# Kernel tuning notes

Measured on AMD Instinct MI355X. Metric: run time of the kernel, lower is better.

Reference implementation:

```python
import jax, jax.numpy as jnp
import numpy as np

N_HEADS = 16
D_MODEL = 1024
NEG_INF = float('-inf')


def _rope_tables(seq_len, d_k, dtype):
    # RoPE(dim=d_k//2): Theta_i = 10000^(-i/dim), repeat-interleaved to width d_k;
    # positions start at 1 (torch uses arange(1, max_len+1)).
    dim = d_k // 2
    theta = jnp.exp(-jnp.arange(dim, dtype=dtype) * (np.log(10000.0) / dim))
    theta = jnp.repeat(theta, 2)                      # [d_k]
    pos = jnp.arange(1, seq_len + 1, dtype=dtype)[:, None]  # [S,1]
    ang = pos * theta                                 # [S,d_k]
    return jnp.sin(ang), jnp.cos(ang)


def _rope(x):
    # x: [B,H,S,d_k]; pair rotation (x0,x1)->(-x1,x0), Rx = x*cos + rot(x)*sin
    B, H, S, d_k = x.shape
    sin, cos = _rope_tables(S, d_k, x.dtype)
    xp = x.reshape(B, H, S, d_k // 2, 2)
    rot = jnp.stack([-xp[..., 1], xp[..., 0]], axis=-1).reshape(x.shape)
    return x * cos + rot * sin


def setup_inputs() -> dict:
    key = jax.random.key(0)
    ks = jax.random.split(key, 8)
    B, S, D, H = 2, 1024, D_MODEL, N_HEADS
    source_query = jax.random.normal(ks[0], (B, S, D), dtype=jnp.float32)
    source_key_value = jax.random.normal(ks[1], (B, S, D), dtype=jnp.float32)
    # tail padding: lengths in [820, 1024]
    q_len = jax.random.randint(ks[2], (B,), 820, S + 1)
    kv_len = jax.random.randint(ks[3], (B,), 820, S + 1)
    pos = jnp.arange(S)
    source_query_padding_mask = pos[None, :] >= q_len[:, None]    # True = pad
    source_key_value_padding_mask = pos[None, :] >= kv_len[:, None]
    prev = jax.random.normal(ks[4], (1, B, H, S, S), dtype=jnp.float32) * 0.5
    Wq = jax.random.normal(ks[5], (D, D), dtype=jnp.float32) * 0.02
    Wk = jax.random.normal(ks[6], (D, D), dtype=jnp.float32) * 0.02
    kv2 = jax.random.split(ks[7], 2)
    Wv = jax.random.normal(kv2[0], (D, D), dtype=jnp.float32) * 0.02
    Wproj = jax.random.normal(kv2[1], (D, D), dtype=jnp.float32) * 0.02
    return dict(source_query=source_query, source_key_value=source_key_value,
                source_query_padding_mask=source_query_padding_mask,
                source_key_value_padding_mask=source_key_value_padding_mask,
                prev=prev, Wq=Wq, Wk=Wk, Wv=Wv, Wproj=Wproj)


def reference(source_query, source_key_value, source_query_padding_mask,
              source_key_value_padding_mask, prev, Wq, Wk, Wv, Wproj):
    B, Sq, D = source_query.shape
    Sk = source_key_value.shape[1]
    H = N_HEADS
    d_k = D // H

    def split_heads(x, S):
        return x.reshape(B, S, H, d_k).transpose(0, 2, 1, 3)  # [B,H,S,d_k]

    # nn.Linear(bias=False): y = x @ W.T
    q = split_heads(jnp.einsum('bsd,ed->bse', source_query, Wq), Sq)
    k = split_heads(jnp.einsum('bsd,ed->bse', source_key_value, Wk), Sk)
    v = split_heads(jnp.einsum('bsd,ed->bse', source_key_value, Wv), Sk)

    q = _rope(q)
    k = _rope(k)

    scores = jnp.einsum('bhqd,bhkd->bhqk', q, k) * (d_k ** -0.5)
    q_pad = source_query_padding_mask[:, None, :, None]   # [B,1,Sq,1]
    kv_pad = source_key_value_padding_mask[:, None, None, :]  # [B,1,1,Sk]
    scores = jnp.where(q_pad, NEG_INF, scores)
    scores = jnp.where(kv_pad, NEG_INF, scores)
    causal = jnp.tril(jnp.ones((Sq, Sq), dtype=bool))      # masked=True
    scores = jnp.where(causal, scores, NEG_INF)

    prev_new = jnp.concatenate([prev, scores[None]], axis=0)  # [L+1,B,H,Sq,Sk]
    avg = prev_new.mean(0)

    # rows fully -inf (padded queries) would softmax to NaN in torch, then get
    # filled with 0 -> compute a safe softmax and zero those rows instead.
    safe = jnp.where(q_pad, 0.0, avg)
    w = jax.nn.softmax(safe, axis=-1)
    w = jnp.where(q_pad, 0.0, w)

    attn = jnp.einsum('bhqk,bhkd->bhqd', w, v)
    attn = attn.transpose(0, 2, 1, 3).reshape(B, Sq, D)
    out = jnp.einsum('bsd,ed->bse', attn, Wproj)  # dropout=0 (eval)
    return out, prev_new
```

## Files before the change

### kernel.cpp

```cpp
#include <hip/hip_runtime.h>
#include <math.h>

#define NSEQ 1024
#define NH   16
#define DKH  64

#define NEGBIG (-1.0e30f)

__global__ __launch_bounds__(256) void normalize_masks(
    const unsigned char* __restrict__ qm, const unsigned char* __restrict__ km,
    int* __restrict__ outq, int* __restrict__ outk)
{
    __shared__ int flag;
    if (threadIdx.x == 0) flag = 0;
    __syncthreads();
    int f = 0;
    for (int i = threadIdx.x; i < 2048; i += 256) {
        if ((i & 3) && qm[i]) f = 1;
        if ((i & 3) && km[i]) f = 1;
    }
    if (f) atomicOr(&flag, 1);
    __syncthreads();
    const int isbyte = flag;
    for (int i = threadIdx.x; i < 2048; i += 256) {
        outq[i] = isbyte ? (int)qm[i] : ((const int*)qm)[i];
        outk[i] = isbyte ? (int)km[i] : ((const int*)km)[i];
    }
}

__device__ __forceinline__ void gemm_core(
    const float* __restrict__ X, const float* __restrict__ W,
    float (*As)[68], float (*Bs)[132], float (&acc)[8][4],
    int m0, int e0, int tid)
{
    const int tm = tid >> 5, tn = tid & 31;
    const int arow = tid >> 2, akq = (tid & 3) * 4;
    const int brow = tid >> 1, bkq = (tid & 1) * 8;
    const float* aptr = &X[(size_t)(m0 + arow) * 1024 + akq];
    const float* bptr = &W[(size_t)(e0 + brow) * 1024 + bkq];

    float4 ar  = *(const float4*)aptr;
    float4 br0 = *(const float4*)bptr;
    float4 br1 = *(const float4*)(bptr + 4);

    for (int k0 = 0; k0 < 1024; k0 += 16) {
        As[akq + 0][arow] = ar.x;  As[akq + 1][arow] = ar.y;
        As[akq + 2][arow] = ar.z;  As[akq + 3][arow] = ar.w;
        Bs[bkq + 0][brow] = br0.x; Bs[bkq + 1][brow] = br0.y;
        Bs[bkq + 2][brow] = br0.z; Bs[bkq + 3][brow] = br0.w;
        Bs[bkq + 4][brow] = br1.x; Bs[bkq + 5][brow] = br1.y;
        Bs[bkq + 6][brow] = br1.z; Bs[bkq + 7][brow] = br1.w;
        __syncthreads();
        if (k0 + 16 < 1024) {
            ar  = *(const float4*)(aptr + k0 + 16);
            br0 = *(const float4*)(bptr + k0 + 16);
            br1 = *(const float4*)(bptr + k0 + 16 + 4);
        }
        #pragma unroll
        for (int k = 0; k < 16; ++k) {
            float a[8], bb[4];
            *(float4*)&a[0]  = *(const float4*)&As[k][tm * 8];
            *(float4*)&a[4]  = *(const float4*)&As[k][tm * 8 + 4];
            *(float4*)&bb[0] = *(const float4*)&Bs[k][tn * 4];
            #pragma unroll
            for (int i = 0; i < 8; ++i)
                #pragma unroll
                for (int j = 0; j < 4; ++j)
                    acc[i][j] += a[i] * bb[j];
        }
        __syncthreads();
    }
}

__global__ __launch_bounds__(256) void gemm_qkv(
    const float* __restrict__ srcq, const float* __restrict__ srckv,
    const float* __restrict__ Wq, const float* __restrict__ Wk,
    const float* __restrict__ Wv,
    float* __restrict__ qh, float* __restrict__ kh, float* __restrict__ vh)
{
    __shared__ float As[16][68];
    __shared__ float Bs[16][132];
    const int tid = threadIdx.x;
    const int z = blockIdx.z;
    const float* X = (z == 0) ? srcq : srckv;
    const float* W = (z == 0) ? Wq : (z == 1) ? Wk : Wv;
    float* Y       = (z == 0) ? qh : (z == 1) ? kh : vh;
    const int m0 = blockIdx.y * 64, e0 = blockIdx.x * 128;

    float acc[8][4] = {{0.f}};
    gemm_core(X, W, As, Bs, acc, m0, e0, tid);

    const int tm = tid >> 5, tn = tid & 31;
    const int col = e0 + tn * 4;
    const int h = col >> 6, dbase = col & 63;
    const bool rope = (z != 2);
    float th0 = 0.f, th1 = 0.f;
    if (rope) {
        const float cth = 0.28782313662425575f;
        th0 = expf(-(float)(dbase >> 1) * cth);
        th1 = expf(-(float)((dbase >> 1) + 1) * cth);
    }
    #pragma unroll
    for (int i = 0; i < 8; ++i) {
        const int m = m0 + tm * 8 + i;
        const int b = m >> 10, s = m & 1023;
        float v0 = acc[i][0], v1 = acc[i][1], v2 = acc[i][2], v3 = acc[i][3];
        if (rope) {
            const float pos = (float)(s + 1);
            float s0, c0, s1, c1;
            sincosf(pos * th0, &s0, &c0);
            sincosf(pos * th1, &s1, &c1);
            float r0 = v0 * c0 - v1 * s0;
            float r1 = v1 * c0 + v0 * s0;
            float r2 = v2 * c1 - v3 * s1;
            float r3 = v3 * c1 + v2 * s1;
            v0 = r0; v1 = r1; v2 = r2; v3 = r3;
        }
        const size_t idx = (((size_t)(b * NH + h) << 10) + s) * DKH + dbase;
        *(float4*)&Y[idx] = make_float4(v0, v1, v2, v3);
    }
}

__global__ __launch_bounds__(256) void gemm_proj(
    const float* __restrict__ X, const float* __restrict__ W,
    float* __restrict__ Y)
{
    __shared__ float As[16][68];
    __shared__ float Bs[16][132];
    const int tid = threadIdx.x;
    const int m0 = blockIdx.y * 64, e0 = blockIdx.x * 128;
    float acc[8][4] = {{0.f}};
    gemm_core(X, W, As, Bs, acc, m0, e0, tid);
    const int tm = tid >> 5, tn = tid & 31;
    #pragma unroll
    for (int i = 0; i < 8; ++i)
        *(float4*)&Y[(size_t)(m0 + tm * 8 + i) * 1024 + e0 + tn * 4] =
            make_float4(acc[i][0], acc[i][1], acc[i][2], acc[i][3]);
}

__global__ __launch_bounds__(256) void flash_fused(
    const float* __restrict__ qh, const float* __restrict__ kh,
    const float* __restrict__ vh, const float* __restrict__ prev,
    const int* __restrict__ nmq, const int* __restrict__ nmk,
    float* __restrict__ prevc, float* __restrict__ scb,
    float* __restrict__ attn)
{
    const int bh = blockIdx.y;
    const int b = bh >> 4, h = bh & 15;
    const int bx = blockIdx.x;
    const int qt = (bx & 1) ? (15 - (bx >> 1)) : (bx >> 1);
    const int q0 = qt * 64;
    const int tid = threadIdx.x;
    const int ti = tid >> 4, tj = tid & 15;
    const int r0 = ti * 4, c0 = tj * 4;
    const size_t base = ((size_t)bh << 10) * 1024;
    const float NI = NEGBIG;

    __shared__ float Qs[64][68];
    __shared__ float KW[64][68];
    __shared__ float Vs[64][68];

    const int lr = tid >> 2;
    const int ld0 = (tid & 3) * 4;
    {
        const float* qbase = qh + (((size_t)bh << 10) + q0) * DKH;
        #pragma unroll
        for (int dq = 0; dq < 4; ++dq) {
            const int d0 = ld0 + dq * 16;
            float4 qv = *(const float4*)&qbase[(size_t)lr * DKH + d0];
            Qs[d0 + 0][lr] = qv.x; Qs[d0 + 1][lr] = qv.y;
            Qs[d0 + 2][lr] = qv.z; Qs[d0 + 3][lr] = qv.w;
        }
    }

    {
        const float4 ninf4 = make_float4(NI, NI, NI, NI);
        for (int kt = qt + 1; kt < 16; ++kt) {
            const int k0 = kt * 64;
            #pragma unroll
            for (int u = 0; u < 4; ++u) {
                const int e = u * 256 + tid;
                const int rr = e >> 4, cc = (e & 15) * 4;
                const size_t idx = base + (size_t)(q0 + rr) * 1024 + k0 + cc;
                *(float4*)&prevc[idx] = *(const float4*)&prev[idx];
                *(float4*)&scb[idx] = ninf4;
            }
        }
    }

    int qmv[4];
    #pragma unroll
    for (int i = 0; i < 4; ++i) qmv[i] = nmq[(b << 10) + q0 + r0 + i];

    float m_i[4], l_i[4], O[4][4];
    #pragma unroll
    for (int i = 0; i < 4; ++i) {
        m_i[i] = -3.0e38f; l_i[i] = 0.f;
        #pragma unroll
        for (int j = 0; j < 4; ++j) O[i][j] = 0.f;
    }

    const float* kbase = kh + ((size_t)bh << 10) * DKH;
    const float* vbase = vh + ((size_t)bh << 10) * DKH;

    for (int kt = 0; kt <= qt; ++kt) {
        const int k0 = kt * 64;
        __syncthreads();

        #pragma unroll
        for (int dq = 0; dq < 4; ++dq) {
            const int d0 = ld0 + dq * 16;
            float4 kv4 = *(const float4*)&kbase[(size_t)(k0 + lr) * DKH + d0];
            KW[d0 + 0][lr] = kv4.x; KW[d0 + 1][lr] = kv4.y;
            KW[d0 + 2][lr] = kv4.z; KW[d0 + 3][lr] = kv4.w;
        }
        #pragma unroll
        for (int u = 0; u < 4; ++u) {
            const int e = u * 256 + tid;
            const int kv = e >> 4, dd = (e & 15) * 4;
            *(float4*)&Vs[kv][dd] =
                *(const float4*)&vbase[(size_t)(k0 + kv) * DKH + dd];
        }
        __syncthreads();

        float acc[4][4] = {{0.f}};
        #pragma unroll 8
        for (int d = 0; d < 64; ++d) {
            float a[4], bb[4];
            *(float4*)a  = *(const float4*)&Qs[d][r0];
            *(float4*)bb = *(const float4*)&KW[d][c0];
            #pragma unroll
            for (int i = 0; i < 4; ++i)
                #pragma unroll
                for (int j = 0; j < 4; ++j)
                    acc[i][j] += a[i] * bb[j];
        }

        int km[4];
        #pragma unroll
        for (int j = 0; j < 4; ++j) km[j] = nmk[(b << 10) + k0 + c0 + j];
        float aw[4][4], tmx[4];
        #pragma unroll
        for (int i = 0; i < 4; ++i) {
            const int row = q0 + r0 + i;
            float o[4];
            #pragma unroll
            for (int j = 0; j < 4; ++j) {
                const int col = k0 + c0 + j;
                const bool masked = (col > row) || (qmv[i] != 0) || (km[j] != 0);
                o[j] = masked ? NI : acc[i][j] * 0.125f;
            }
            const size_t idx = base + (size_t)row * 1024 + k0 + c0;
            *(float4*)&scb[idx] = make_float4(o[0], o[1], o[2], o[3]);
            const float4 p4 = *(const float4*)&prev[idx];
            *(float4*)&prevc[idx] = p4;
            aw[i][0] = 0.5f * (p4.x + o[0]);
            aw[i][1] = 0.5f * (p4.y + o[1]);
            aw[i][2] = 0.5f * (p4.z + o[2]);
            aw[i][3] = 0.5f * (p4.w + o[3]);
            tmx[i] = fmaxf(fmaxf(aw[i][0], aw[i][1]), fmaxf(aw[i][2], aw[i][3]));
        }
        #pragma unroll
        for (int i = 0; i < 4; ++i)
            #pragma unroll
            for (int off = 1; off < 16; off <<= 1)
                tmx[i] = fmaxf(tmx[i], __shfl_xor(tmx[i], off));

        __syncthreads();

        #pragma unroll
        for (int i = 0; i < 4; ++i) {
            const float mn = fmaxf(m_i[i], tmx[i]);
            const float fac = expf(m_i[i] - mn);
            m_i[i] = mn;
            float w0 = expf(aw[i][0] - mn);
            float w1 = expf(aw[i][1] - mn);
            float w2 = expf(aw[i][2] - mn);
            float w3 = expf(aw[i][3] - mn);
            float sl = w0 + w1 + w2 + w3;
            #pragma unroll
            for (int off = 1; off < 16; off <<= 1)
                sl += __shfl_xor(sl, off);
            l_i[i] = l_i[i] * fac + sl;
            #pragma unroll
            for (int j = 0; j < 4; ++j) O[i][j] *= fac;
            KW[c0 + 0][r0 + i] = w0;
            KW[c0 + 1][r0 + i] = w1;
            KW[c0 + 2][r0 + i] = w2;
            KW[c0 + 3][r0 + i] = w3;
        }
        __syncthreads();

        #pragma unroll 8
        for (int k = 0; k < 64; ++k) {
            float wv[4], vv[4];
            *(float4*)wv = *(const float4*)&KW[k][r0];
            *(float4*)vv = *(const float4*)&Vs[k][c0];
            #pragma unroll
            for (int i = 0; i < 4; ++i)
                #pragma unroll
                for (int j = 0; j < 4; ++j)
                    O[i][j] += wv[i] * vv[j];
        }
    }

    #pragma unroll
    for (int i = 0; i < 4; ++i) {
        const int q = q0 + r0 + i;
        const float inv = qmv[i] ? 0.f : 1.f / l_i[i];
        float4 o4 = make_float4(O[i][0] * inv, O[i][1] * inv,
                                O[i][2] * inv, O[i][3] * inv);
        *(float4*)&attn[(size_t)((b << 10) + q) * 1024 + (h << 6) + c0] = o4;
    }
}

extern "C" void kernel_launch(void* const* d_in, const int* in_sizes, int n_in,
                              void* d_out, int out_size, void* d_ws, size_t ws_size,
                              hipStream_t stream) {
    const float* srcq  = (const float*)d_in[0];
    const float* srckv = (const float*)d_in[1];
    const void*  qmask = d_in[2];
    const void*  kmask = d_in[3];
    const float* prev  = (const float*)d_in[4];
    const float* Wq    = (const float*)d_in[5];
    const float* Wk    = (const float*)d_in[6];
    const float* Wv    = (const float*)d_in[7];
    const float* Wp    = (const float*)d_in[8];

    float* out0  = (float*)d_out;
    float* prevc = out0 + 2097152;
    float* scb   = prevc + 33554432;

    float* qh   = (float*)d_ws;
    float* kh   = qh + 2097152;
    float* vh   = kh + 2097152;
    float* attn = vh + 2097152;
    int*   nmq  = (int*)(attn + 2097152);
    int*   nmk  = nmq + 2048;

    hipLaunchKernelGGL(normalize_masks, dim3(1), dim3(256), 0, stream,
                       (const unsigned char*)qmask, (const unsigned char*)kmask, nmq, nmk);
    hipLaunchKernelGGL(gemm_qkv, dim3(8, 32, 3), dim3(256), 0, stream,
                       srcq, srckv, Wq, Wk, Wv, qh, kh, vh);
    hipLaunchKernelGGL(flash_fused, dim3(16, 32), dim3(256), 0, stream,
                       qh, kh, vh, prev, nmq, nmk, prevc, scb, attn);
    hipLaunchKernelGGL(gemm_proj, dim3(8, 32), dim3(256), 0, stream,
                       attn, Wp, out0);
}
```

Before: 727.2 us.

## Use split-bf16 MFMA for QKV and output projection GEMMs

Replaces the FP32 SIMT GEMM core with an MFMA-based core. Each FP32 input is split into bf16 high and low parts, and three bf16 MFMAs (hi*hi, hi*lo, lo*hi) are accumulated to approximate FP32 precision. Tiles change to 128x64 with a bf16 LDS layout, and the RoPE epilogue is rewritten for the MFMA output layout using a lane shuffle. The goal is to move the projection GEMMs onto the matrix cores, at the cost of extra conversion work, scalar global stores, and slightly reduced precision.

```diff
diff --git a/kernel.cpp b/kernel.cpp
--- a/kernel.cpp
+++ b/kernel.cpp
@@ -6,6 +6,11 @@
 #define DKH  64
 
 #define NEGBIG (-1.0e30f)
+
+typedef unsigned short u16;
+typedef unsigned int   u32;
+typedef __attribute__((ext_vector_type(8))) short short8;
+typedef __attribute__((ext_vector_type(4))) float f32x4;
 
 __global__ __launch_bounds__(256) void normalize_masks(
     const unsigned char* __restrict__ qm, const unsigned char* __restrict__ km,
@@ -28,47 +33,85 @@
     }
 }
 
-__device__ __forceinline__ void gemm_core(
+__device__ __forceinline__ u32 bf16_rn(float x) {
+    u32 u = __float_as_uint(x);
+    return (u + 0x7FFFu + ((u >> 16) & 1u)) >> 16;
+}
+__device__ __forceinline__ void bf16_split(float x, u32 &h, u32 &l) {
+    h = bf16_rn(x);
+    l = bf16_rn(x - __uint_as_float(h << 16));
+}
+
+__device__ __forceinline__ void mfma_core(
     const float* __restrict__ X, const float* __restrict__ W,
-    float (*As)[68], float (*Bs)[132], float (&acc)[8][4],
-    int m0, int e0, int tid)
+    u16 (*Ahi)[40], u16 (*Alo)[40], u16 (*Bhi)[40], u16 (*Blo)[40],
+    f32x4 (&acc)[4][2], int m0, int e0, int tid)
 {
-    const int tm = tid >> 5, tn = tid & 31;
-    const int arow = tid >> 2, akq = (tid & 3) * 4;
-    const int brow = tid >> 1, bkq = (tid & 1) * 8;
-    const float* aptr = &X[(size_t)(m0 + arow) * 1024 + akq];
-    const float* bptr = &W[(size_t)(e0 + brow) * 1024 + bkq];
-
-    float4 ar  = *(const float4*)aptr;
-    float4 br0 = *(const float4*)bptr;
-    float4 br1 = *(const float4*)(bptr + 4);
-
-    for (int k0 = 0; k0 < 1024; k0 += 16) {
-        As[akq + 0][arow] = ar.x;  As[akq + 1][arow] = ar.y;
-        As[akq + 2][arow] = ar.z;  As[akq + 3][arow] = ar.w;
-        Bs[bkq + 0][brow] = br0.x; Bs[bkq + 1][brow] = br0.y;
-        Bs[bkq + 2][brow] = br0.z; Bs[bkq + 3][brow] = br0.w;
-        Bs[bkq + 4][brow] = br1.x; Bs[bkq + 5][brow] = br1.y;
-        Bs[bkq + 6][brow] = br1.z; Bs[bkq + 7][brow] = br1.w;
-        __syncthreads();
-        if (k0 + 16 < 1024) {
-            ar  = *(const float4*)(aptr + k0 + 16);
-            br0 = *(const float4*)(bptr + k0 + 16);
-            br1 = *(const float4*)(bptr + k0 + 16 + 4);
-        }
-        #pragma unroll
-        for (int k = 0; k < 16; ++k) {
-            float a[8], bb[4];
-            *(float4*)&a[0]  = *(const float4*)&As[k][tm * 8];
-            *(float4*)&a[4]  = *(const float4*)&As[k][tm * 8 + 4];
-            *(float4*)&bb[0] = *(const float4*)&Bs[k][tn * 4];
-            #pragma unroll
-            for (int i = 0; i < 8; ++i)
-                #pragma unroll
-                for (int j = 0; j < 4; ++j)
-                    acc[i][j] += a[i] * bb[j];
-        }
-        __syncthreads();
+    const int lane = tid & 63, wid = tid >> 6;
+    const int wm = wid >> 1, wn = wid & 1;
+    const int l15 = lane & 15, lq = lane >> 4;
+    const int arow = tid >> 1, aks = (tid & 1) * 16;
+    const int brow = tid >> 2, bks = (tid & 3) * 8;
+    const float* aptr = &X[(size_t)(m0 + arow) * 1024 + aks];
+    const float* bptr = &W[(size_t)(e0 + brow) * 1024 + bks];
+
+    float4 xa[4], xb[2];
+    #pragma unroll
+    for (int c = 0; c < 4; ++c) xa[c] = *(const float4*)(aptr + 4 * c);
+    #pragma unroll
+    for (int c = 0; c < 2; ++c) xb[c] = *(const float4*)(bptr + 4 * c);
+
+    for (int k0 = 0; k0 < 1024; k0 += 32) {
+        u32 pah[8], pal[8], pbh[4], pbl[4];
+        #pragma unroll
+        for (int c = 0; c < 4; ++c) {
+            u32 h0, l0, h1, l1, h2, l2, h3, l3;
+            bf16_split(xa[c].x, h0, l0); bf16_split(xa[c].y, h1, l1);
+            bf16_split(xa[c].z, h2, l2); bf16_split(xa[c].w, h3, l3);
+            pah[2 * c] = h0 | (h1 << 16); pah[2 * c + 1] = h2 | (h3 << 16);
+            pal[2 * c] = l0 | (l1 << 16); pal[2 * c + 1] = l2 | (l3 << 16);
+        }
+        #pragma unroll
+        for (int c = 0; c < 2; ++c) {
+            u32 h0, l0, h1, l1, h2, l2, h3, l3;
+            bf16_split(xb[c].x, h0, l0); bf16_split(xb[c].y, h1, l1);
+            bf16_split(xb[c].z, h2, l2); bf16_split(xb[c].w, h3, l3);
+            pbh[2 * c] = h0 | (h1 << 16); pbh[2 * c + 1] = h2 | (h3 << 16);
+            pbl[2 * c] = l0 | (l1 << 16); pbl[2 * c + 1] = l2 | (l3 << 16);
+        }
+        __syncthreads();
+        *(uint4*)&Ahi[arow][aks]     = make_uint4(pah[0], pah[1], pah[2], pah[3]);
+        *(uint4*)&Ahi[arow][aks + 8] = make_uint4(pah[4], pah[5], pah[6], pah[7]);
+        *(uint4*)&Alo[arow][aks]     = make_uint4(pal[0], pal[1], pal[2], pal[3]);
+        *(uint4*)&Alo[arow][aks + 8] = make_uint4(pal[4], pal[5], pal[6], pal[7]);
+        *(uint4*)&Bhi[brow][bks]     = make_uint4(pbh[0], pbh[1], pbh[2], pbh[3]);
+        *(uint4*)&Blo[brow][bks]     = make_uint4(pbl[0], pbl[1], pbl[2], pbl[3]);
+        __syncthreads();
+        if (k0 + 32 < 1024) {
+            #pragma unroll
+            for (int c = 0; c < 4; ++c) xa[c] = *(const float4*)(aptr + k0 + 32 + 4 * c);
+            #pragma unroll
+            for (int c = 0; c < 2; ++c) xb[c] = *(const float4*)(bptr + k0 + 32 + 4 * c);
+        }
+        short8 bh8[2], bl8[2];
+        #pragma unroll
+        for (int fn = 0; fn < 2; ++fn) {
+            const int bc = wn * 32 + fn * 16 + l15;
+            bh8[fn] = *(const short8*)&Bhi[bc][lq * 8];
+            bl8[fn] = *(const short8*)&Blo[bc][lq * 8];
+        }
+        #pragma unroll
+        for (int fm = 0; fm < 4; ++fm) {
+            const int ar = wm * 64 + fm * 16 + l15;
+            short8 ah8 = *(const short8*)&Ahi[ar][lq * 8];
+            short8 al8 = *(const short8*)&Alo[ar][lq * 8];
+            #pragma unroll
+            for (int fn = 0; fn < 2; ++fn) {
+                acc[fm][fn] = __builtin_amdgcn_mfma_f32_16x16x32_bf16(ah8, bh8[fn], acc[fm][fn], 0, 0, 0);
+                acc[fm][fn] = __builtin_amdgcn_mfma_f32_16x16x32_bf16(ah8, bl8[fn], acc[fm][fn], 0, 0, 0);
+                acc[fm][fn] = __builtin_amdgcn_mfma_f32_16x16x32_bf16(al8, bh8[fn], acc[fm][fn], 0, 0, 0);
+            }
+        }
     }
 }
 
@@ -78,46 +121,57 @@
     const float* __restrict__ Wv,
     float* __restrict__ qh, float* __restrict__ kh, float* __restrict__ vh)
 {
-    __shared__ float As[16][68];
-    __shared__ float Bs[16][132];
+    __shared__ __align__(16) u16 Ahi[128][40];
+    __shared__ __align__(16) u16 Alo[128][40];
+    __shared__ __align__(16) u16 Bhi[64][40];
+    __shared__ __align__(16) u16 Blo[64][40];
     const int tid = threadIdx.x;
     const int z = blockIdx.z;
     const float* X = (z == 0) ? srcq : srckv;
     const float* W = (z == 0) ? Wq : (z == 1) ? Wk : Wv;
     float* Y       = (z == 0) ? qh : (z == 1) ? kh : vh;
-    const int m0 = blockIdx.y * 64, e0 = blockIdx.x * 128;
-
-    float acc[8][4] = {{0.f}};
-    gemm_core(X, W, As, Bs, acc, m0, e0, tid);
-
-    const int tm = tid >> 5, tn = tid & 31;
-    const int col = e0 + tn * 4;
-    const int h = col >> 6, dbase = col & 63;
+    const int m0 = blockIdx.y * 128, e0 = blockIdx.x * 64;
+
+    f32x4 acc[4][2];
+    #pragma unroll
+    for (int i = 0; i < 4; ++i)
+        #pragma unroll
+        for (int j = 0; j < 2; ++j) acc[i][j] = (f32x4){0.f, 0.f, 0.f, 0.f};
+
+    mfma_core(X, W, Ahi, Alo, Bhi, Blo, acc, m0, e0, tid);
+
+    const int lane = tid & 63, wid = tid >> 6;
+    const int wm = wid >> 1, wn = wid & 1;
+    const int l15 = lane & 15, lq = lane >> 4;
     const bool rope = (z != 2);
-    float th0 = 0.f, th1 = 0.f;
-    if (rope) {
-        const float cth = 0.28782313662425575f;
-        th0 = expf(-(float)(dbase >> 1) * cth);
-        th1 = expf(-(float)((dbase >> 1) + 1) * cth);
-    }
-    #pragma unroll
-    for (int i = 0; i < 8; ++i) {
-        const int m = m0 + tm * 8 + i;
-        const int b = m >> 10, s = m & 1023;
-        float v0 = acc[i][0], v1 = acc[i][1], v2 = acc[i][2], v3 = acc[i][3];
-        if (rope) {
+    const float cth = 0.28782313662425575f;
+    float th[2];
+    #pragma unroll
+    for (int fn = 0; fn < 2; ++fn) {
+        const int e = e0 + wn * 32 + fn * 16 + l15;
+        th[fn] = rope ? expf(-(float)((e & 63) >> 1) * cth) : 0.f;
+    }
+    #pragma unroll
+    for (int fm = 0; fm < 4; ++fm) {
+        #pragma unroll
+        for (int r = 0; r < 4; ++r) {
+            const int m = m0 + wm * 64 + fm * 16 + lq * 4 + r;
+            const int b = m >> 10, s = m & 1023;
             const float pos = (float)(s + 1);
-            float s0, c0, s1, c1;
-            sincosf(pos * th0, &s0, &c0);
-            sincosf(pos * th1, &s1, &c1);
-            float r0 = v0 * c0 - v1 * s0;
-            float r1 = v1 * c0 + v0 * s0;
-            float r2 = v2 * c1 - v3 * s1;
-            float r3 = v3 * c1 + v2 * s1;
-            v0 = r0; v1 = r1; v2 = r2; v3 = r3;
-        }
-        const size_t idx = (((size_t)(b * NH + h) << 10) + s) * DKH + dbase;
-        *(float4*)&Y[idx] = make_float4(v0, v1, v2, v3);
+            #pragma unroll
+            for (int fn = 0; fn < 2; ++fn) {
+                const int e = e0 + wn * 32 + fn * 16 + l15;
+                float v = acc[fm][fn][r];
+                const float vp = __shfl_xor(v, 1);
+                if (rope) {
+                    float sp, cp;
+                    sincosf(pos * th[fn], &sp, &cp);
+                    v = (lane & 1) ? (v * cp + vp * sp) : (v * cp - vp * sp);
+                }
+                const int h = e >> 6, db = e & 63;
+                Y[(((size_t)(b * NH + h) << 10) + s) * DKH + db] = v;
+            }
+        }
     }
 }
 
@@ -125,17 +179,36 @@
     const float* __restrict__ X, const float* __restrict__ W,
     float* __restrict__ Y)
 {
-    __shared__ float As[16][68];
-    __shared__ float Bs[16][132];
+    __shared__ __align__(16) u16 Ahi[128][40];
+    __shared__ __align__(16) u16 Alo[128][40];
+    __shared__ __align__(16) u16 Bhi[64][40];
+    __shared__ __align__(16) u16 Blo[64][40];
     const int tid = threadIdx.x;
-    const int m0 = blockIdx.y * 64, e0 = blockIdx.x * 128;
-    float acc[8][4] = {{0.f}};
-    gemm_core(X, W, As, Bs, acc, m0, e0, tid);
-    const int tm = tid >> 5, tn = tid & 31;
-    #pragma unroll
-    for (int i = 0; i < 8; ++i)
-        *(float4*)&Y[(size_t)(m0 + tm * 8 + i) * 1024 + e0 + tn * 4] =
-            make_float4(acc[i][0], acc[i][1], acc[i][2], acc[i][3]);
+    const int m0 = blockIdx.y * 128, e0 = blockIdx.x * 64;
+
+    f32x4 acc[4][2];
+    #pragma unroll
+    for (int i = 0; i < 4; ++i)
+        #pragma unroll
+        for (int j = 0; j < 2; ++j) acc[i][j] = (f32x4){0.f, 0.f, 0.f, 0.f};
+
+    mfma_core(X, W, Ahi, Alo, Bhi, Blo, acc, m0, e0, tid);
+
+    const int lane = tid & 63, wid = tid >> 6;
+    const int wm = wid >> 1, wn = wid & 1;
+    const int l15 = lane & 15, lq = lane >> 4;
+    #pragma unroll
+    for (int fm = 0; fm < 4; ++fm) {
+        #pragma unroll
+        for (int fn = 0; fn < 2; ++fn) {
+            #pragma unroll
+            for (int r = 0; r < 4; ++r) {
+                const int row = m0 + wm * 64 + fm * 16 + lq * 4 + r;
+                const int col = e0 + wn * 32 + fn * 16 + l15;
+                Y[(size_t)row * 1024 + col] = acc[fm][fn][r];
+            }
+        }
+    }
 }
 
 __global__ __launch_bounds__(256) void flash_fused(
@@ -340,10 +413,10 @@
 
     hipLaunchKernelGGL(normalize_masks, dim3(1), dim3(256), 0, stream,
                        (const unsigned char*)qmask, (const unsigned char*)kmask, nmq, nmk);
-    hipLaunchKernelGGL(gemm_qkv, dim3(8, 32, 3), dim3(256), 0, stream,
+    hipLaunchKernelGGL(gemm_qkv, dim3(16, 16, 3), dim3(256), 0, stream,
                        srcq, srckv, Wq, Wk, Wv, qh, kh, vh);
     hipLaunchKernelGGL(flash_fused, dim3(16, 32), dim3(256), 0, stream,
                        qh, kh, vh, prev, nmq, nmk, prevc, scb, attn);
-    hipLaunchKernelGGL(gemm_proj, dim3(8, 32), dim3(256), 0, stream,
+    hipLaunchKernelGGL(gemm_proj, dim3(16, 16), dim3(256), 0, stream,
                        attn, Wp, out0);
 }
```

After: 596.9 us. -17.9%, faster.
